# Optimization experiments

Hardware: AMD Instinct MI355X
Metric: run time of the kernel (lower is better)

The kernel has to match this reference:

```python
import jax, jax.numpy as jnp
import numpy as np

H, K, R, DQ = 128, 128, 512, 1536  # num_heads, head_dim, lora_rank, q_lora_rank
B, L = 32, 4096


def setup_inputs() -> dict:
    key = jax.random.key(0)
    k1, k2, k3, k4, k5, k6 = jax.random.split(key, 6)
    scale_q = 1.0 / np.sqrt(DQ)
    scale_r = 1.0 / np.sqrt(R)
    return {
        "hidden_states_q": jax.random.normal(k1, (B, DQ), jnp.float32),
        "compressed_kv": jax.random.normal(k2, (B, L, R), jnp.float32),
        "Wq": jax.random.normal(k3, (H * K, DQ), jnp.float32) * scale_q,
        "bq": jax.random.normal(k4, (H * K,), jnp.float32) * scale_q,
        "w_kc": jax.random.normal(k5, (H, K, R), jnp.float32) * scale_r,  # k_proj.weight viewed [H,K,R]
        "w_vc": jax.random.normal(k6, (H, K, R), jnp.float32) * scale_r,  # v_proj.weight viewed [H,K,R]
    }


def reference(hidden_states_q, compressed_kv, Wq, bq, w_kc, w_vc):
    bsz = hidden_states_q.shape[0]
    # q_proj: [B, DQ] -> [B, H, K]
    q = (hidden_states_q @ Wq.T + bq).reshape(bsz, H, K)
    # query absorption: w_kc^T @ q  -> [B, H, R]
    q_abs = jnp.einsum('hkr,bhk->bhr', w_kc, q)
    # attention scores over cached latent KV: [B, H, L] (note: no 1/sqrt(d) scaling, as in source)
    scores = jnp.einsum('bhr,blr->bhl', q_abs, compressed_kv)
    probs = jax.nn.softmax(scores, axis=-1)
    # context in latent space: [B, H, R]
    ctx = jnp.einsum('bhl,blr->bhr', probs, compressed_kv)
    # output absorption: w_vc @ ctx -> [B, H, K] -> [B, H*K]
    out = jnp.einsum('hkr,bhr->bhk', w_vc, ctx)
    return out.reshape(bsz, H * K)
```

## Files before the change

### kernel.cpp

```cpp
#include <hip/hip_runtime.h>
#include <hip/hip_fp16.h>
#include <cmath>

#define NH 128
#define HD 128
#define RR 512
#define DQ 1536
#define BB 32
#define LL 4096
#define NSPLIT 8
#define LCHUNK 512
#define LTILE 32
#define NITER 16
#define LOG2E 1.44269504088896340736f

typedef _Float16 f16;
typedef f16 f16x4 __attribute__((ext_vector_type(4)));
typedef f16 f16x8 __attribute__((ext_vector_type(8)));
typedef float f32x4 __attribute__((ext_vector_type(4)));

__global__ __launch_bounds__(256) void qproj_kernel(const float* __restrict__ hidden,
                                                    const float* __restrict__ Wq,
                                                    const float* __restrict__ bq,
                                                    float* __restrict__ q) {
    __shared__ float hid[32][132];
    __shared__ float wqt[128][68];
    const int tid = threadIdx.x;
    const int blk = blockIdx.x;
    const int c0 = (tid & 15) * 4;
    const int rbase = (tid >> 4) * 2;
    float acc[2][4] = {};
    for (int dt = 0; dt < DQ; dt += 128) {
        __syncthreads();
#pragma unroll
        for (int j = 0; j < 4; ++j) {
            int i = j * 256 + tid;
            int b = i >> 5, d4 = (i & 31) * 4;
            *(f32x4*)&hid[b][d4] = *(const f32x4*)&hidden[(size_t)b * DQ + dt + d4];
        }
#pragma unroll
        for (int j = 0; j < 8; ++j) {
            int i = j * 256 + tid;
            int cr = i >> 5, d4 = (i & 31) * 4;
            f32x4 v = *(const f32x4*)&Wq[(size_t)(blk * 64 + cr) * DQ + dt + d4];
            wqt[d4 + 0][cr] = v.x; wqt[d4 + 1][cr] = v.y;
            wqt[d4 + 2][cr] = v.z; wqt[d4 + 3][cr] = v.w;
        }
        __syncthreads();
        for (int kk = 0; kk < 128; ++kk) {
            f32x4 w = *(const f32x4*)&wqt[kk][c0];
            float h0 = hid[rbase][kk], h1 = hid[rbase + 1][kk];
            acc[0][0] += w.x * h0; acc[0][1] += w.y * h0; acc[0][2] += w.z * h0; acc[0][3] += w.w * h0;
            acc[1][0] += w.x * h1; acc[1][1] += w.y * h1; acc[1][2] += w.z * h1; acc[1][3] += w.w * h1;
        }
    }
    const int col = blk * 64 + c0;
    f32x4 bias = *(const f32x4*)&bq[col];
#pragma unroll
    for (int i = 0; i < 2; ++i) {
        f32x4 o;
        o.x = acc[i][0] + bias.x; o.y = acc[i][1] + bias.y;
        o.z = acc[i][2] + bias.z; o.w = acc[i][3] + bias.w;
        *(f32x4*)&q[(size_t)(rbase + i) * (NH * HD) + col] = o;
    }
}

__global__ __launch_bounds__(256) void qabs_kernel(const float* __restrict__ q,
                                                   const float* __restrict__ w_kc,
                                                   f16* __restrict__ qabs) {
    __shared__ float qh[32][132];
    __shared__ float wl[128][68];
    const int tid = threadIdx.x;
    const int h = blockIdx.x >> 1;
    const int r0 = (blockIdx.x & 1) * 256;
#pragma unroll
    for (int j = 0; j < 4; ++j) {
        int i = j * 256 + tid;
        int b = i >> 5, k4 = (i & 31) * 4;
        *(f32x4*)&qh[b][k4] = *(const f32x4*)&q[(size_t)b * (NH * HD) + h * HD + k4];
    }
    const int rg = tid & 15, bg = tid >> 4;
    for (int rt = 0; rt < 4; ++rt) {
        __syncthreads();
#pragma unroll
        for (int j = 0; j < 8; ++j) {
            int i = j * 256 + tid;
            int kk = i >> 4, r4 = (i & 15) * 4;
            *(f32x4*)&wl[kk][r4] =
                *(const f32x4*)&w_kc[((size_t)h * HD + kk) * RR + r0 + rt * 64 + r4];
        }
        __syncthreads();
        float acc[2][4] = {};
        for (int kk = 0; kk < 128; ++kk) {
            f32x4 w = *(const f32x4*)&wl[kk][rg * 4];
            float q0 = qh[bg * 2][kk], q1 = qh[bg * 2 + 1][kk];
            acc[0][0] += w.x * q0; acc[0][1] += w.y * q0; acc[0][2] += w.z * q0; acc[0][3] += w.w * q0;
            acc[1][0] += w.x * q1; acc[1][1] += w.y * q1; acc[1][2] += w.z * q1; acc[1][3] += w.w * q1;
        }
        const int r = r0 + rt * 64 + rg * 4;
#pragma unroll
        for (int i = 0; i < 2; ++i) {
            f16x4 o = {(f16)acc[i][0], (f16)acc[i][1], (f16)acc[i][2], (f16)acc[i][3]};
            *(f16x4*)&qabs[((size_t)(bg * 2 + i) * NH + h) * RR + r] = o;
        }
    }
}

__global__ __launch_bounds__(512, 2) void attn_kernel(const float* __restrict__ ckv,
                                                      const f16* __restrict__ qabs,
                                                      f16* __restrict__ part,
                                                      float* __restrict__ stats) {
    __shared__ f16 kv_lr[LTILE][520];
    __shared__ f16 kv_rl[RR][40];
    __shared__ f16 p_lds[8][16][40];
    const int tid = threadIdx.x;
    const int lane = tid & 63;
    const int wave = tid >> 6;
    const int lh = lane & 15;
    const int quad = lane >> 4;
    const int b = blockIdx.x >> 3;
    const int s = blockIdx.x & 7;
    const int head = wave * 16 + lh;

    f16x8 qf[16];
#pragma unroll
    for (int rc = 0; rc < 16; ++rc)
        qf[rc] = *(const f16x8*)&qabs[((size_t)b * NH + head) * RR + rc * 32 + quad * 8];

    f32x4 acc[32];
#pragma unroll
    for (int rt = 0; rt < 32; ++rt) acc[rt] = f32x4{0.f, 0.f, 0.f, 0.f};
    float m_run = -INFINITY, l_run = 0.0f;

    const f32x4* src = (const f32x4*)(ckv + ((size_t)b * LL + s * LCHUNK) * RR);

    for (int it = 0; it < NITER; ++it) {
        const f32x4* tsrc = src + (size_t)it * (LTILE * RR / 4);
#pragma unroll
        for (int j = 0; j < 8; ++j) {
            int idx = j * 512 + tid;
            f32x4 v = tsrc[idx];
            int l = idx >> 7, r4 = (idx & 127) * 4;
            f16 h0 = (f16)v.x, h1 = (f16)v.y, h2 = (f16)v.z, h3 = (f16)v.w;
            f16x4 pk = {h0, h1, h2, h3};
            *(f16x4*)&kv_lr[l][r4] = pk;
            kv_rl[r4 + 0][l] = h0;
            kv_rl[r4 + 1][l] = h1;
            kv_rl[r4 + 2][l] = h2;
            kv_rl[r4 + 3][l] = h3;
        }
        __syncthreads();
        f32x4 sc[2];
#pragma unroll
        for (int lt = 0; lt < 2; ++lt) {
            f32x4 s4 = f32x4{0.f, 0.f, 0.f, 0.f};
#pragma unroll
            for (int rc = 0; rc < 16; ++rc) {
                f16x8 a = *(const f16x8*)&kv_lr[lt * 16 + lh][rc * 32 + quad * 8];
                s4 = __builtin_amdgcn_mfma_f32_16x16x32_f16(a, qf[rc], s4, 0, 0, 0);
            }
            sc[lt] = s4;
        }
        float tmax = fmaxf(fmaxf(fmaxf(sc[0].x, sc[0].y), fmaxf(sc[0].z, sc[0].w)),
                           fmaxf(fmaxf(sc[1].x, sc[1].y), fmaxf(sc[1].z, sc[1].w)));
        tmax = fmaxf(tmax, __shfl_xor(tmax, 16, 64));
        tmax = fmaxf(tmax, __shfl_xor(tmax, 32, 64));
        float new_m = fmaxf(m_run, tmax);
        float alpha = exp2f((m_run - new_m) * LOG2E);
        float p0 = exp2f((sc[0].x - new_m) * LOG2E);
        float p1 = exp2f((sc[0].y - new_m) * LOG2E);
        float p2 = exp2f((sc[0].z - new_m) * LOG2E);
        float p3 = exp2f((sc[0].w - new_m) * LOG2E);
        float p4 = exp2f((sc[1].x - new_m) * LOG2E);
        float p5 = exp2f((sc[1].y - new_m) * LOG2E);
        float p6 = exp2f((sc[1].z - new_m) * LOG2E);
        float p7 = exp2f((sc[1].w - new_m) * LOG2E);
        f16x4 pk0 = {(f16)p0, (f16)p1, (f16)p2, (f16)p3};
        f16x4 pk1 = {(f16)p4, (f16)p5, (f16)p6, (f16)p7};
        *(f16x4*)&p_lds[wave][lh][quad * 4] = pk0;
        *(f16x4*)&p_lds[wave][lh][16 + quad * 4] = pk1;
        float psum = p0 + p1 + p2 + p3 + p4 + p5 + p6 + p7;
        psum += __shfl_xor(psum, 16, 64);
        psum += __shfl_xor(psum, 32, 64);
        l_run = l_run * alpha + psum;
        m_run = new_m;
        f16x8 pb = *(const f16x8*)&p_lds[wave][lh][quad * 8];
#pragma unroll
        for (int rt = 0; rt < 32; ++rt) {
            f16x8 a = *(const f16x8*)&kv_rl[rt * 16 + lh][quad * 8];
            f32x4 c = acc[rt];
            c.x *= alpha; c.y *= alpha; c.z *= alpha; c.w *= alpha;
            acc[rt] = __builtin_amdgcn_mfma_f32_16x16x32_f16(a, pb, c, 0, 0, 0);
        }
        __syncthreads();
    }
    float inv_l = 1.0f / l_run;
    size_t base = (((size_t)b * NSPLIT + s) * NH + head) * RR;
#pragma unroll
    for (int rt = 0; rt < 32; ++rt) {
        f16x4 o = {(f16)(acc[rt].x * inv_l), (f16)(acc[rt].y * inv_l),
                   (f16)(acc[rt].z * inv_l), (f16)(acc[rt].w * inv_l)};
        *(f16x4*)&part[base + rt * 16 + quad * 4] = o;
    }
    if (quad == 0) {
        size_t sb = (((size_t)b * NSPLIT + s) * NH + head) * 2;
        stats[sb] = m_run;
        stats[sb + 1] = l_run;
    }
}

__global__ __launch_bounds__(128) void combine_kernel(const f16* __restrict__ part,
                                                      const float* __restrict__ stats,
                                                      float* __restrict__ ctx) {
    const int blk = blockIdx.x;
    const int b = blk >> 7, h = blk & 127;
    const int tid = threadIdx.x;
    float m[NSPLIT], l[NSPLIT];
    float M = -INFINITY;
#pragma unroll
    for (int s = 0; s < NSPLIT; ++s) {
        size_t sb = (((size_t)b * NSPLIT + s) * NH + h) * 2;
        m[s] = stats[sb]; l[s] = stats[sb + 1];
        M = fmaxf(M, m[s]);
    }
    float w[NSPLIT], denom = 0.f;
#pragma unroll
    for (int s = 0; s < NSPLIT; ++s) {
        w[s] = l[s] * exp2f((m[s] - M) * LOG2E);
        denom += w[s];
    }
    float inv = 1.0f / denom;
    f32x4 sum = f32x4{0.f, 0.f, 0.f, 0.f};
#pragma unroll
    for (int s = 0; s < NSPLIT; ++s) {
        f16x4 v = *(const f16x4*)&part[(((size_t)b * NSPLIT + s) * NH + h) * RR + tid * 4];
        sum.x += w[s] * (float)v.x; sum.y += w[s] * (float)v.y;
        sum.z += w[s] * (float)v.z; sum.w += w[s] * (float)v.w;
    }
    sum.x *= inv; sum.y *= inv; sum.z *= inv; sum.w *= inv;
    *(f32x4*)&ctx[((size_t)b * NH + h) * RR + tid * 4] = sum;
}

__global__ __launch_bounds__(256) void outproj_kernel(const float* __restrict__ ctx,
                                                      const float* __restrict__ w_vc,
                                                      float* __restrict__ out) {
    __shared__ float cl[32][524];
    __shared__ float wl[64][69];
    const int tid = threadIdx.x;
    const int h = blockIdx.x >> 1;
    const int k0 = (blockIdx.x & 1) * 64;
#pragma unroll
    for (int j = 0; j < 16; ++j) {
        int i = j * 256 + tid;
        int bb = i >> 7, r4 = (i & 127) * 4;
        *(f32x4*)&cl[bb][r4] = *(const f32x4*)&ctx[((size_t)bb * NH + h) * RR + r4];
    }
    const int kg = tid & 15, bg = tid >> 4;
    float acc[2][4] = {};
    for (int rt = 0; rt < 8; ++rt) {
        __syncthreads();
#pragma unroll
        for (int j = 0; j < 4; ++j) {
            int i = j * 256 + tid;
            int kk = i >> 4, r4 = (i & 15) * 4;
            f32x4 v = *(const f32x4*)&w_vc[((size_t)h * HD + k0 + kk) * RR + rt * 64 + r4];
            wl[kk][r4 + 0] = v.x; wl[kk][r4 + 1] = v.y;
            wl[kk][r4 + 2] = v.z; wl[kk][r4 + 3] = v.w;
        }
        __syncthreads();
        for (int rr = 0; rr < 64; ++rr) {
            float c0 = cl[bg * 2][rt * 64 + rr], c1 = cl[bg * 2 + 1][rt * 64 + rr];
            float w0 = wl[kg * 4 + 0][rr], w1 = wl[kg * 4 + 1][rr];
            float w2 = wl[kg * 4 + 2][rr], w3 = wl[kg * 4 + 3][rr];
            acc[0][0] += w0 * c0; acc[0][1] += w1 * c0; acc[0][2] += w2 * c0; acc[0][3] += w3 * c0;
            acc[1][0] += w0 * c1; acc[1][1] += w1 * c1; acc[1][2] += w2 * c1; acc[1][3] += w3 * c1;
        }
    }
#pragma unroll
    for (int i = 0; i < 2; ++i) {
        f32x4 o = {acc[i][0], acc[i][1], acc[i][2], acc[i][3]};
        *(f32x4*)&out[(size_t)(bg * 2 + i) * (NH * HD) + h * HD + k0 + kg * 4] = o;
    }
}

extern "C" void kernel_launch(void* const* d_in, const int* in_sizes, int n_in,
                              void* d_out, int out_size, void* d_ws, size_t ws_size,
                              hipStream_t stream) {
    const float* hidden = (const float*)d_in[0];
    const float* ckv    = (const float*)d_in[1];
    const float* Wq     = (const float*)d_in[2];
    const float* bq     = (const float*)d_in[3];
    const float* w_kc   = (const float*)d_in[4];
    const float* w_vc   = (const float*)d_in[5];
    float* out = (float*)d_out;

    char* ws = (char*)d_ws;
    float* q     = (float*)(ws);
    f16*   qabs  = (f16*)(ws + 2097152);
    f16*   part  = (f16*)(ws + 6291456);
    float* stats = (float*)(ws + 39845888);
    float* ctx   = (float*)(ws + 40108032);

    qproj_kernel<<<256, 256, 0, stream>>>(hidden, Wq, bq, q);
    qabs_kernel<<<256, 256, 0, stream>>>(q, w_kc, qabs);
    attn_kernel<<<256, 512, 0, stream>>>(ckv, qabs, part, stats);
    combine_kernel<<<BB * NH, 128, 0, stream>>>(part, stats, ctx);
    outproj_kernel<<<256, 256, 0, stream>>>(ctx, w_vc, out);
}
```

Before: 601.4 us.

## Move projections to fp16 MFMA and prefetch KV tiles in attention

Rewrites the q-projection, query-absorption and output-projection kernels to convert their inputs to fp16 in shared memory and use 16x16x32 MFMA instead of scalar FP32 FMA loops. Intermediates q and ctx are stored in fp16. The attention kernel now prefetches the next KV tile into registers while it computes on the current one, transposes into the R-major buffer with packed stores and a narrower pad, and stages partial outputs through LDS so global writes are coalesced. This cuts ALU time in the small GEMMs and hides some KV load latency, at the cost of extra fp16 rounding and higher register pressure.

```diff
diff --git a/kernel.cpp b/kernel.cpp
--- a/kernel.cpp
+++ b/kernel.cpp
@@ -19,91 +19,109 @@
 typedef f16 f16x8 __attribute__((ext_vector_type(8)));
 typedef float f32x4 __attribute__((ext_vector_type(4)));
 
-__global__ __launch_bounds__(256) void qproj_kernel(const float* __restrict__ hidden,
+__global__ __launch_bounds__(512) void qproj_kernel(const float* __restrict__ hidden,
                                                     const float* __restrict__ Wq,
                                                     const float* __restrict__ bq,
-                                                    float* __restrict__ q) {
-    __shared__ float hid[32][132];
-    __shared__ float wqt[128][68];
-    const int tid = threadIdx.x;
-    const int blk = blockIdx.x;
-    const int c0 = (tid & 15) * 4;
-    const int rbase = (tid >> 4) * 2;
-    float acc[2][4] = {};
+                                                    f16* __restrict__ q16) {
+    __shared__ f16 wq_s[64][136];
+    __shared__ f16 hid_s[32][136];
+    const int tid = threadIdx.x;
+    const int lane = tid & 63, wave = tid >> 6;
+    const int lh = lane & 15, quad = lane >> 4;
+    const int mt = wave & 1, nt = wave >> 1;
+    const int col0 = blockIdx.x * 64;
+    f32x4 acc = {0.f, 0.f, 0.f, 0.f};
     for (int dt = 0; dt < DQ; dt += 128) {
         __syncthreads();
-#pragma unroll
-        for (int j = 0; j < 4; ++j) {
-            int i = j * 256 + tid;
-            int b = i >> 5, d4 = (i & 31) * 4;
-            *(f32x4*)&hid[b][d4] = *(const f32x4*)&hidden[(size_t)b * DQ + dt + d4];
-        }
-#pragma unroll
-        for (int j = 0; j < 8; ++j) {
-            int i = j * 256 + tid;
-            int cr = i >> 5, d4 = (i & 31) * 4;
-            f32x4 v = *(const f32x4*)&Wq[(size_t)(blk * 64 + cr) * DQ + dt + d4];
-            wqt[d4 + 0][cr] = v.x; wqt[d4 + 1][cr] = v.y;
-            wqt[d4 + 2][cr] = v.z; wqt[d4 + 3][cr] = v.w;
+        {
+            int r = tid >> 3, sg = (tid & 7) * 16;
+            const float* src = &Wq[(size_t)(col0 + r) * DQ + dt + sg];
+            f32x4 a0 = *(const f32x4*)&src[0], a1 = *(const f32x4*)&src[4];
+            f32x4 a2 = *(const f32x4*)&src[8], a3 = *(const f32x4*)&src[12];
+            f16x8 p0 = {(f16)a0.x,(f16)a0.y,(f16)a0.z,(f16)a0.w,(f16)a1.x,(f16)a1.y,(f16)a1.z,(f16)a1.w};
+            f16x8 p1 = {(f16)a2.x,(f16)a2.y,(f16)a2.z,(f16)a2.w,(f16)a3.x,(f16)a3.y,(f16)a3.z,(f16)a3.w};
+            *(f16x8*)&wq_s[r][sg] = p0;
+            *(f16x8*)&wq_s[r][sg + 8] = p1;
+        }
+        {
+            int r = tid >> 4, sg = (tid & 15) * 8;
+            const float* src = &hidden[(size_t)r * DQ + dt + sg];
+            f32x4 b0 = *(const f32x4*)&src[0], b1 = *(const f32x4*)&src[4];
+            f16x8 p = {(f16)b0.x,(f16)b0.y,(f16)b0.z,(f16)b0.w,(f16)b1.x,(f16)b1.y,(f16)b1.z,(f16)b1.w};
+            *(f16x8*)&hid_s[r][sg] = p;
         }
         __syncthreads();
-        for (int kk = 0; kk < 128; ++kk) {
-            f32x4 w = *(const f32x4*)&wqt[kk][c0];
-            float h0 = hid[rbase][kk], h1 = hid[rbase + 1][kk];
-            acc[0][0] += w.x * h0; acc[0][1] += w.y * h0; acc[0][2] += w.z * h0; acc[0][3] += w.w * h0;
-            acc[1][0] += w.x * h1; acc[1][1] += w.y * h1; acc[1][2] += w.z * h1; acc[1][3] += w.w * h1;
-        }
-    }
-    const int col = blk * 64 + c0;
-    f32x4 bias = *(const f32x4*)&bq[col];
-#pragma unroll
-    for (int i = 0; i < 2; ++i) {
-        f32x4 o;
-        o.x = acc[i][0] + bias.x; o.y = acc[i][1] + bias.y;
-        o.z = acc[i][2] + bias.z; o.w = acc[i][3] + bias.w;
-        *(f32x4*)&q[(size_t)(rbase + i) * (NH * HD) + col] = o;
-    }
-}
-
-__global__ __launch_bounds__(256) void qabs_kernel(const float* __restrict__ q,
+#pragma unroll
+        for (int kk = 0; kk < 4; ++kk) {
+            f16x8 a = *(const f16x8*)&hid_s[mt * 16 + lh][kk * 32 + quad * 8];
+            f16x8 bb = *(const f16x8*)&wq_s[nt * 16 + lh][kk * 32 + quad * 8];
+            acc = __builtin_amdgcn_mfma_f32_16x16x32_f16(a, bb, acc, 0, 0, 0);
+        }
+    }
+    const int col = col0 + nt * 16 + lh;
+    const float bias = bq[col];
+#pragma unroll
+    for (int i = 0; i < 4; ++i)
+        q16[(size_t)(mt * 16 + quad * 4 + i) * (NH * HD) + col] = (f16)(acc[i] + bias);
+}
+
+__global__ __launch_bounds__(512) void qabs_kernel(const f16* __restrict__ q16,
                                                    const float* __restrict__ w_kc,
                                                    f16* __restrict__ qabs) {
-    __shared__ float qh[32][132];
-    __shared__ float wl[128][68];
-    const int tid = threadIdx.x;
+    __shared__ f16 wk_s[256][136];
+    __shared__ f16 q_s[32][136];
+    const int tid = threadIdx.x;
+    const int lane = tid & 63, wave = tid >> 6;
+    const int lh = lane & 15, quad = lane >> 4;
     const int h = blockIdx.x >> 1;
-    const int r0 = (blockIdx.x & 1) * 256;
-#pragma unroll
-    for (int j = 0; j < 4; ++j) {
-        int i = j * 256 + tid;
-        int b = i >> 5, k4 = (i & 31) * 4;
-        *(f32x4*)&qh[b][k4] = *(const f32x4*)&q[(size_t)b * (NH * HD) + h * HD + k4];
-    }
-    const int rg = tid & 15, bg = tid >> 4;
-    for (int rt = 0; rt < 4; ++rt) {
-        __syncthreads();
-#pragma unroll
-        for (int j = 0; j < 8; ++j) {
-            int i = j * 256 + tid;
-            int kk = i >> 4, r4 = (i & 15) * 4;
-            *(f32x4*)&wl[kk][r4] =
-                *(const f32x4*)&w_kc[((size_t)h * HD + kk) * RR + r0 + rt * 64 + r4];
-        }
-        __syncthreads();
-        float acc[2][4] = {};
-        for (int kk = 0; kk < 128; ++kk) {
-            f32x4 w = *(const f32x4*)&wl[kk][rg * 4];
-            float q0 = qh[bg * 2][kk], q1 = qh[bg * 2 + 1][kk];
-            acc[0][0] += w.x * q0; acc[0][1] += w.y * q0; acc[0][2] += w.z * q0; acc[0][3] += w.w * q0;
-            acc[1][0] += w.x * q1; acc[1][1] += w.y * q1; acc[1][2] += w.z * q1; acc[1][3] += w.w * q1;
-        }
-        const int r = r0 + rt * 64 + rg * 4;
-#pragma unroll
-        for (int i = 0; i < 2; ++i) {
-            f16x4 o = {(f16)acc[i][0], (f16)acc[i][1], (f16)acc[i][2], (f16)acc[i][3]};
-            *(f16x4*)&qabs[((size_t)(bg * 2 + i) * NH + h) * RR + r] = o;
-        }
-    }
+    const int rh = blockIdx.x & 1;
+    {
+        int bb = tid >> 4, sg = (tid & 15) * 8;
+        *(f16x8*)&q_s[bb][sg] = *(const f16x8*)&q16[(size_t)bb * (NH * HD) + h * HD + sg];
+    }
+    {
+        int k0 = (tid & 31) * 4, rb = tid >> 5;
+#pragma unroll
+        for (int j3 = 0; j3 < 2; ++j3) {
+            int r0 = rb * 8 + j3 * 128;
+            f16 ha[4][8];
+#pragma unroll
+            for (int ki = 0; ki < 4; ++ki) {
+                const float* src = &w_kc[((size_t)h * HD + k0 + ki) * RR + rh * 256 + r0];
+                f32x4 v0 = *(const f32x4*)&src[0], v1 = *(const f32x4*)&src[4];
+                ha[ki][0]=(f16)v0.x; ha[ki][1]=(f16)v0.y; ha[ki][2]=(f16)v0.z; ha[ki][3]=(f16)v0.w;
+                ha[ki][4]=(f16)v1.x; ha[ki][5]=(f16)v1.y; ha[ki][6]=(f16)v1.z; ha[ki][7]=(f16)v1.w;
+            }
+#pragma unroll
+            for (int j = 0; j < 8; ++j) {
+                f16x4 c = {ha[0][j], ha[1][j], ha[2][j], ha[3][j]};
+                *(f16x4*)&wk_s[r0 + j][k0] = c;
+            }
+        }
+    }
+    __syncthreads();
+    f32x4 acc[2][2] = {};
+#pragma unroll
+    for (int kt = 0; kt < 4; ++kt) {
+        f16x8 a0 = *(const f16x8*)&q_s[lh][kt * 32 + quad * 8];
+        f16x8 a1 = *(const f16x8*)&q_s[16 + lh][kt * 32 + quad * 8];
+#pragma unroll
+        for (int j = 0; j < 2; ++j) {
+            f16x8 bb = *(const f16x8*)&wk_s[(wave * 2 + j) * 16 + lh][kt * 32 + quad * 8];
+            acc[0][j] = __builtin_amdgcn_mfma_f32_16x16x32_f16(a0, bb, acc[0][j], 0, 0, 0);
+            acc[1][j] = __builtin_amdgcn_mfma_f32_16x16x32_f16(a1, bb, acc[1][j], 0, 0, 0);
+        }
+    }
+#pragma unroll
+    for (int m = 0; m < 2; ++m)
+#pragma unroll
+        for (int j = 0; j < 2; ++j)
+#pragma unroll
+            for (int i = 0; i < 4; ++i) {
+                int b = m * 16 + quad * 4 + i;
+                int r = rh * 256 + (wave * 2 + j) * 16 + lh;
+                qabs[((size_t)b * NH + h) * RR + r] = (f16)acc[m][j][i];
+            }
 }
 
 __global__ __launch_bounds__(512, 2) void attn_kernel(const float* __restrict__ ckv,
@@ -111,13 +129,11 @@
                                                       f16* __restrict__ part,
                                                       float* __restrict__ stats) {
     __shared__ f16 kv_lr[LTILE][520];
-    __shared__ f16 kv_rl[RR][40];
+    __shared__ f16 kv_rl[RR][36];
     __shared__ f16 p_lds[8][16][40];
     const int tid = threadIdx.x;
-    const int lane = tid & 63;
-    const int wave = tid >> 6;
-    const int lh = lane & 15;
-    const int quad = lane >> 4;
+    const int lane = tid & 63, wave = tid >> 6;
+    const int lh = lane & 15, quad = lane >> 4;
     const int b = blockIdx.x >> 3;
     const int s = blockIdx.x & 7;
     const int head = wave * 16 + lh;
@@ -132,24 +148,44 @@
     for (int rt = 0; rt < 32; ++rt) acc[rt] = f32x4{0.f, 0.f, 0.f, 0.f};
     float m_run = -INFINITY, l_run = 0.0f;
 
-    const f32x4* src = (const f32x4*)(ckv + ((size_t)b * LL + s * LCHUNK) * RR);
+    const int rb = tid >> 3;
+    const int l0 = (tid & 7) * 4;
+    const float* base = ckv + ((size_t)b * LL + s * LCHUNK) * RR;
+
+    f32x4 pv[4][2];
+#pragma unroll
+    for (int li = 0; li < 4; ++li) {
+        pv[li][0] = *(const f32x4*)&base[(size_t)(l0 + li) * RR + rb * 8];
+        pv[li][1] = *(const f32x4*)&base[(size_t)(l0 + li) * RR + rb * 8 + 4];
+    }
 
     for (int it = 0; it < NITER; ++it) {
-        const f32x4* tsrc = src + (size_t)it * (LTILE * RR / 4);
+        f16 ha[4][8];
+#pragma unroll
+        for (int li = 0; li < 4; ++li) {
+            f32x4 v0 = pv[li][0], v1 = pv[li][1];
+            ha[li][0]=(f16)v0.x; ha[li][1]=(f16)v0.y; ha[li][2]=(f16)v0.z; ha[li][3]=(f16)v0.w;
+            ha[li][4]=(f16)v1.x; ha[li][5]=(f16)v1.y; ha[li][6]=(f16)v1.z; ha[li][7]=(f16)v1.w;
+        }
+#pragma unroll
+        for (int li = 0; li < 4; ++li) {
+            f16x8 row = {ha[li][0],ha[li][1],ha[li][2],ha[li][3],ha[li][4],ha[li][5],ha[li][6],ha[li][7]};
+            *(f16x8*)&kv_lr[l0 + li][rb * 8] = row;
+        }
 #pragma unroll
         for (int j = 0; j < 8; ++j) {
-            int idx = j * 512 + tid;
-            f32x4 v = tsrc[idx];
-            int l = idx >> 7, r4 = (idx & 127) * 4;
-            f16 h0 = (f16)v.x, h1 = (f16)v.y, h2 = (f16)v.z, h3 = (f16)v.w;
-            f16x4 pk = {h0, h1, h2, h3};
-            *(f16x4*)&kv_lr[l][r4] = pk;
-            kv_rl[r4 + 0][l] = h0;
-            kv_rl[r4 + 1][l] = h1;
-            kv_rl[r4 + 2][l] = h2;
-            kv_rl[r4 + 3][l] = h3;
+            f16x4 c = {ha[0][j], ha[1][j], ha[2][j], ha[3][j]};
+            *(f16x4*)&kv_rl[rb * 8 + j][l0] = c;
         }
         __syncthreads();
+        if (it + 1 < NITER) {
+            const float* nb = base + (size_t)(it + 1) * LTILE * RR;
+#pragma unroll
+            for (int li = 0; li < 4; ++li) {
+                pv[li][0] = *(const f32x4*)&nb[(size_t)(l0 + li) * RR + rb * 8];
+                pv[li][1] = *(const f32x4*)&nb[(size_t)(l0 + li) * RR + rb * 8 + 4];
+            }
+        }
         f32x4 sc[2];
 #pragma unroll
         for (int lt = 0; lt < 2; ++lt) {
@@ -187,7 +223,9 @@
         f16x8 pb = *(const f16x8*)&p_lds[wave][lh][quad * 8];
 #pragma unroll
         for (int rt = 0; rt < 32; ++rt) {
-            f16x8 a = *(const f16x8*)&kv_rl[rt * 16 + lh][quad * 8];
+            f16x4 alo = *(const f16x4*)&kv_rl[rt * 16 + lh][quad * 8];
+            f16x4 ahi = *(const f16x4*)&kv_rl[rt * 16 + lh][quad * 8 + 4];
+            f16x8 a = __builtin_shufflevector(alo, ahi, 0, 1, 2, 3, 4, 5, 6, 7);
             f32x4 c = acc[rt];
             c.x *= alpha; c.y *= alpha; c.z *= alpha; c.w *= alpha;
             acc[rt] = __builtin_amdgcn_mfma_f32_16x16x32_f16(a, pb, c, 0, 0, 0);
@@ -195,12 +233,22 @@
         __syncthreads();
     }
     float inv_l = 1.0f / l_run;
-    size_t base = (((size_t)b * NSPLIT + s) * NH + head) * RR;
-#pragma unroll
-    for (int rt = 0; rt < 32; ++rt) {
-        f16x4 o = {(f16)(acc[rt].x * inv_l), (f16)(acc[rt].y * inv_l),
-                   (f16)(acc[rt].z * inv_l), (f16)(acc[rt].w * inv_l)};
-        *(f16x4*)&part[base + rt * 16 + quad * 4] = o;
+    f16* ebuf = (f16*)kv_rl + wave * (16 * 136);
+    const int h2 = lane >> 2, off = (lane & 3) * 32;
+    size_t obase = (((size_t)b * NSPLIT + s) * NH + wave * 16) * RR;
+#pragma unroll
+    for (int c = 0; c < 4; ++c) {
+#pragma unroll
+        for (int rt2 = 0; rt2 < 8; ++rt2) {
+            f32x4 v = acc[c * 8 + rt2];
+            f16x4 o = {(f16)(v.x * inv_l), (f16)(v.y * inv_l), (f16)(v.z * inv_l), (f16)(v.w * inv_l)};
+            *(f16x4*)&ebuf[lh * 136 + rt2 * 16 + quad * 4] = o;
+        }
+#pragma unroll
+        for (int k2 = 0; k2 < 4; ++k2) {
+            f16x8 v = *(const f16x8*)&ebuf[h2 * 136 + off + k2 * 8];
+            *(f16x8*)&part[obase + (size_t)h2 * RR + c * 128 + off + k2 * 8] = v;
+        }
     }
     if (quad == 0) {
         size_t sb = (((size_t)b * NSPLIT + s) * NH + head) * 2;
@@ -211,7 +259,7 @@
 
 __global__ __launch_bounds__(128) void combine_kernel(const f16* __restrict__ part,
                                                       const float* __restrict__ stats,
-                                                      float* __restrict__ ctx) {
+                                                      f16* __restrict__ ctx) {
     const int blk = blockIdx.x;
     const int b = blk >> 7, h = blk & 127;
     const int tid = threadIdx.x;
@@ -237,50 +285,49 @@
         sum.x += w[s] * (float)v.x; sum.y += w[s] * (float)v.y;
         sum.z += w[s] * (float)v.z; sum.w += w[s] * (float)v.w;
     }
-    sum.x *= inv; sum.y *= inv; sum.z *= inv; sum.w *= inv;
-    *(f32x4*)&ctx[((size_t)b * NH + h) * RR + tid * 4] = sum;
-}
-
-__global__ __launch_bounds__(256) void outproj_kernel(const float* __restrict__ ctx,
+    f16x4 o = {(f16)(sum.x * inv), (f16)(sum.y * inv), (f16)(sum.z * inv), (f16)(sum.w * inv)};
+    *(f16x4*)&ctx[((size_t)b * NH + h) * RR + tid * 4] = o;
+}
+
+__global__ __launch_bounds__(512) void outproj_kernel(const f16* __restrict__ ctx,
                                                       const float* __restrict__ w_vc,
                                                       float* __restrict__ out) {
-    __shared__ float cl[32][524];
-    __shared__ float wl[64][69];
-    const int tid = threadIdx.x;
+    __shared__ f16 wv_s[64][520];
+    __shared__ f16 ctx_s[32][520];
+    const int tid = threadIdx.x;
+    const int lane = tid & 63, wave = tid >> 6;
+    const int lh = lane & 15, quad = lane >> 4;
     const int h = blockIdx.x >> 1;
-    const int k0 = (blockIdx.x & 1) * 64;
-#pragma unroll
-    for (int j = 0; j < 16; ++j) {
-        int i = j * 256 + tid;
-        int bb = i >> 7, r4 = (i & 127) * 4;
-        *(f32x4*)&cl[bb][r4] = *(const f32x4*)&ctx[((size_t)bb * NH + h) * RR + r4];
-    }
-    const int kg = tid & 15, bg = tid >> 4;
-    float acc[2][4] = {};
-    for (int rt = 0; rt < 8; ++rt) {
-        __syncthreads();
-#pragma unroll
-        for (int j = 0; j < 4; ++j) {
-            int i = j * 256 + tid;
-            int kk = i >> 4, r4 = (i & 15) * 4;
-            f32x4 v = *(const f32x4*)&w_vc[((size_t)h * HD + k0 + kk) * RR + rt * 64 + r4];
-            wl[kk][r4 + 0] = v.x; wl[kk][r4 + 1] = v.y;
-            wl[kk][r4 + 2] = v.z; wl[kk][r4 + 3] = v.w;
-        }
-        __syncthreads();
-        for (int rr = 0; rr < 64; ++rr) {
-            float c0 = cl[bg * 2][rt * 64 + rr], c1 = cl[bg * 2 + 1][rt * 64 + rr];
-            float w0 = wl[kg * 4 + 0][rr], w1 = wl[kg * 4 + 1][rr];
-            float w2 = wl[kg * 4 + 2][rr], w3 = wl[kg * 4 + 3][rr];
-            acc[0][0] += w0 * c0; acc[0][1] += w1 * c0; acc[0][2] += w2 * c0; acc[0][3] += w3 * c0;
-            acc[1][0] += w0 * c1; acc[1][1] += w1 * c1; acc[1][2] += w2 * c1; acc[1][3] += w3 * c1;
-        }
-    }
-#pragma unroll
-    for (int i = 0; i < 2; ++i) {
-        f32x4 o = {acc[i][0], acc[i][1], acc[i][2], acc[i][3]};
-        *(f32x4*)&out[(size_t)(bg * 2 + i) * (NH * HD) + h * HD + k0 + kg * 4] = o;
-    }
+    const int kh = blockIdx.x & 1;
+    {
+        int bb = tid >> 4, sg = (tid & 15) * 32;
+        const f16* src = &ctx[((size_t)bb * NH + h) * RR + sg];
+#pragma unroll
+        for (int k2 = 0; k2 < 4; ++k2)
+            *(f16x8*)&ctx_s[bb][sg + k2 * 8] = *(const f16x8*)&src[k2 * 8];
+    }
+    {
+        int r = tid >> 3, sg = (tid & 7) * 64;
+        const float* src = &w_vc[((size_t)h * HD + kh * 64 + r) * RR + sg];
+#pragma unroll
+        for (int u = 0; u < 8; ++u) {
+            f32x4 v0 = *(const f32x4*)&src[u * 8], v1 = *(const f32x4*)&src[u * 8 + 4];
+            f16x8 p = {(f16)v0.x,(f16)v0.y,(f16)v0.z,(f16)v0.w,(f16)v1.x,(f16)v1.y,(f16)v1.z,(f16)v1.w};
+            *(f16x8*)&wv_s[r][sg + u * 8] = p;
+        }
+    }
+    __syncthreads();
+    const int mt = wave & 1, nt = wave >> 1;
+    f32x4 acc = {0.f, 0.f, 0.f, 0.f};
+#pragma unroll
+    for (int kt = 0; kt < 16; ++kt) {
+        f16x8 a = *(const f16x8*)&ctx_s[mt * 16 + lh][kt * 32 + quad * 8];
+        f16x8 bb = *(const f16x8*)&wv_s[nt * 16 + lh][kt * 32 + quad * 8];
+        acc = __builtin_amdgcn_mfma_f32_16x16x32_f16(a, bb, acc, 0, 0, 0);
+    }
+#pragma unroll
+    for (int i = 0; i < 4; ++i)
+        out[(size_t)(mt * 16 + quad * 4 + i) * (NH * HD) + h * HD + kh * 64 + nt * 16 + lh] = acc[i];
 }
 
 extern "C" void kernel_launch(void* const* d_in, const int* in_sizes, int n_in,
@@ -295,15 +342,15 @@
     float* out = (float*)d_out;
 
     char* ws = (char*)d_ws;
-    float* q     = (float*)(ws);
-    f16*   qabs  = (f16*)(ws + 2097152);
-    f16*   part  = (f16*)(ws + 6291456);
-    float* stats = (float*)(ws + 39845888);
-    float* ctx   = (float*)(ws + 40108032);
-
-    qproj_kernel<<<256, 256, 0, stream>>>(hidden, Wq, bq, q);
-    qabs_kernel<<<256, 256, 0, stream>>>(q, w_kc, qabs);
+    f16*   q16   = (f16*)(ws);
+    f16*   qabs  = (f16*)(ws + (1u << 20));
+    f16*   part  = (f16*)(ws + 5u * (1u << 20));
+    float* stats = (float*)(ws + 37u * (1u << 20));
+    f16*   ctx   = (f16*)(ws + 38u * (1u << 20));
+
+    qproj_kernel<<<256, 512, 0, stream>>>(hidden, Wq, bq, q16);
+    qabs_kernel<<<256, 512, 0, stream>>>(q16, w_kc, qabs);
     attn_kernel<<<256, 512, 0, stream>>>(ckv, qabs, part, stats);
     combine_kernel<<<BB * NH, 128, 0, stream>>>(part, stats, ctx);
-    outproj_kernel<<<256, 256, 0, stream>>>(ctx, w_vc, out);
-}
+    outproj_kernel<<<256, 512, 0, stream>>>(ctx, w_vc, out);
+}
```

After: 539.0 us. 10.4% less time.
